# Kernel tuning notes

Measured on AMD Instinct MI355X. Metric: run time of the kernel, lower is better.

Reference implementation:

```python
import math
import jax, jax.numpy as jnp
import numpy as np

B, L, D = 2, 2048, 2048
H, DH = 16, 128
DFF = 8192


def setup_inputs() -> dict:
    key = jax.random.key(0)
    ks = jax.random.split(key, 9)
    x = jax.random.normal(ks[0], (B, L, D), dtype=jnp.float32)
    # additive causal mask: 0 on/below diagonal, -inf above
    neg = jnp.finfo(jnp.float32).min
    mask = jnp.where(jnp.tril(jnp.ones((L, L), dtype=bool)), 0.0, neg)[None, None]
    s = 0.02
    return {
        "x": x,
        "mask": mask,
        "ln1_w": jnp.ones((D,), jnp.float32),
        "wq": jax.random.normal(ks[1], (D, D), jnp.float32) * s,
        "wk": jax.random.normal(ks[2], (D, D), jnp.float32) * s,
        "wv": jax.random.normal(ks[3], (D, D), jnp.float32) * s,
        "wo": jax.random.normal(ks[4], (D, D), jnp.float32) * s,
        "ln2_w": jnp.ones((D,), jnp.float32),
        "w_up": jax.random.normal(ks[5], (DFF, D), jnp.float32) * s,
        "w_down": jax.random.normal(ks[6], (D, DFF), jnp.float32) * s,
    }


def _rmsnorm(x, w, eps=1e-8):
    rms = jnp.sqrt(jnp.mean(x * x, axis=-1, keepdims=True) + eps)
    return x / rms * w


def reference(x, mask, ln1_w, wq, wk, wv, wo, ln2_w, w_up, w_down):
    h = _rmsnorm(x, ln1_w)
    # torch Linear: y = x @ W.T ; weights are [out, in]
    q = (h @ wq.T).reshape(B, L, H, DH).transpose(0, 2, 1, 3)  # [B,H,L,DH]
    k = (h @ wk.T).reshape(B, L, H, DH).transpose(0, 2, 1, 3)
    v = (h @ wv.T).reshape(B, L, H, DH).transpose(0, 2, 1, 3)
    scores = jnp.einsum('bhqd,bhkd->bhqk', q, k) / math.sqrt(DH)
    scores = scores + mask
    attn = jax.nn.softmax(scores, axis=-1)
    out = jnp.einsum('bhqk,bhkd->bhqd', attn, v)
    out = out.transpose(0, 2, 1, 3).reshape(B, L, D)
    x = x + out @ wo.T
    h = _rmsnorm(x, ln2_w)
    ff = jax.nn.gelu(h @ w_up.T, approximate=False) @ w_down.T  # exact erf GELU as in F.gelu
    return x + ff
```

## Files before the change

### kernel.cpp

```cpp
#include <hip/hip_runtime.h>
#include <hip/hip_bf16.h>
#include <math.h>

#define B_   2
#define L_   2048
#define D_   2048
#define H_   16
#define DH_  128
#define DFF_ 8192
#define NTOK (B_*L_)

typedef __attribute__((ext_vector_type(8))) short bf16x8;
typedef __attribute__((ext_vector_type(4))) float floatx4;
typedef unsigned short u16;

__device__ __forceinline__ u16 f2bf(float f) {
    union { float f; unsigned u; } c; c.f = f;
    unsigned r = (c.u + 0x7fffu + ((c.u >> 16) & 1u)) >> 16;
    return (u16)r;
}

__device__ __forceinline__ void async_cp16(const u16* g, u16* l) {
    __builtin_amdgcn_global_load_lds(
        (const __attribute__((address_space(1))) unsigned int*)g,
        (__attribute__((address_space(3))) unsigned int*)l,
        16, 0, 0);
}

__global__ __launch_bounds__(256) void cvt_bf16(const float* __restrict__ in,
                                                u16* __restrict__ out, int n4) {
    int i = blockIdx.x * 256 + threadIdx.x;
    if (i >= n4) return;
    float4 v = ((const float4*)in)[i];
    ushort4 o = { f2bf(v.x), f2bf(v.y), f2bf(v.z), f2bf(v.w) };
    ((ushort4*)out)[i] = o;
}

__global__ __launch_bounds__(256) void rmsnorm_kernel(const float* __restrict__ x,
                                                      const float* __restrict__ w,
                                                      u16* __restrict__ out) {
    const int row = blockIdx.x, tid = threadIdx.x;
    const float* xr = x + (size_t)row * D_;
    float4 a = ((const float4*)xr)[tid];
    float4 b = ((const float4*)xr)[tid + 256];
    float ss = a.x*a.x + a.y*a.y + a.z*a.z + a.w*a.w
             + b.x*b.x + b.y*b.y + b.z*b.z + b.w*b.w;
#pragma unroll
    for (int d = 1; d < 64; d <<= 1) ss += __shfl_xor(ss, d, 64);
    __shared__ float sred[4];
    if ((tid & 63) == 0) sred[tid >> 6] = ss;
    __syncthreads();
    float tot = sred[0] + sred[1] + sred[2] + sred[3];
    float inv = 1.0f / sqrtf(tot * (1.0f / D_) + 1e-8f);
    float4 w0 = ((const float4*)w)[tid];
    float4 w1 = ((const float4*)w)[tid + 256];
    ushort4 o0 = { f2bf(a.x*inv*w0.x), f2bf(a.y*inv*w0.y), f2bf(a.z*inv*w0.z), f2bf(a.w*inv*w0.w) };
    ushort4 o1 = { f2bf(b.x*inv*w1.x), f2bf(b.y*inv*w1.y), f2bf(b.z*inv*w1.z), f2bf(b.w*inv*w1.w) };
    ushort4* orow = (ushort4*)(out + (size_t)row * D_);
    orow[tid] = o0;
    orow[tid + 256] = o1;
}


template<int MODE>
__global__ __launch_bounds__(512, 2) void gemm256(const u16* __restrict__ A,
                                                  const u16* __restrict__ Bw,
                                                  void* __restrict__ outp,
                                                  void* __restrict__ outp2,
                                                  const float* __restrict__ residual,
                                                  int M, int N, int K, float scale) {
    __shared__ __attribute__((aligned(16))) u16 lds_a[2][256 * 64];
    __shared__ __attribute__((aligned(16))) u16 lds_b[2][256 * 64];
    const int tid = threadIdx.x;
    const int wave = tid >> 6, lane = tid & 63;
    const int qd = lane >> 4, c16 = lane & 15;
    const int wm = wave >> 2, wn = wave & 3;
    const int gx = gridDim.x;
    const int nwg = gx * gridDim.y;
    const int orig = blockIdx.y * gx + blockIdx.x;
    const int id2 = (orig & 7) * (nwg >> 3) + (orig >> 3);
    const long tile_m = (long)(id2 / gx) * 256, tile_n = (long)(id2 % gx) * 256;
    const int NT = K >> 6;

    const int srow = tid >> 3;
    const int scol = (((tid & 7) ^ (srow & 7))) * 8;
    const u16* Asrc = A + (tile_m + srow) * (long)K + scol;
    const u16* Bsrc = Bw + (tile_n + srow) * (long)K + scol;
    const int stoff = tid * 8;

#define STAGE_A2(bi, g0, g1, ko) do { \
        async_cp16(Asrc + (long)(g0) * 64 * K + (ko), &lds_a[bi][(g0) * 4096 + stoff]); \
        async_cp16(Asrc + (long)(g1) * 64 * K + (ko), &lds_a[bi][(g1) * 4096 + stoff]); \
    } while (0)
#define STAGE_B2(bi, g0, g1, ko) do { \
        async_cp16(Bsrc + (long)(g0) * 64 * K + (ko), &lds_b[bi][(g0) * 4096 + stoff]); \
        async_cp16(Bsrc + (long)(g1) * 64 * K + (ko), &lds_b[bi][(g1) * 4096 + stoff]); \
    } while (0)

    const int csw = (qd * 16) ^ ((c16 & 7) << 4);
    const int arowb = (wm * 128 + c16) * 128;
    const int browb = (wn * 64 + c16) * 128;
#define LDAF(bi, i, ks) (*(const bf16x8*)((const char*)&lds_a[bi][0] + arowb + (i) * 2048 + (csw ^ ((ks) * 64))))
#define LDBF(bi, j, ks) (*(const bf16x8*)((const char*)&lds_b[bi][0] + browb + (j) * 2048 + (csw ^ ((ks) * 64))))
#define MFMA_(a, b, c) __builtin_amdgcn_mfma_f32_16x16x32_bf16(a, b, c, 0, 0, 0)

    floatx4 acc[8][4] = {};

    STAGE_B2(0, 0, 1, 0); STAGE_B2(0, 2, 3, 0);
    STAGE_A2(0, 0, 2, 0); STAGE_A2(0, 1, 3, 0);
    STAGE_B2(1, 0, 1, 64); STAGE_B2(1, 2, 3, 64);
    STAGE_A2(1, 0, 2, 64);
    asm volatile("s_waitcnt vmcnt(6)" ::: "memory");
    __builtin_amdgcn_s_barrier();
    asm volatile("" ::: "memory");

    bf16x8 bfr[4][2];

#define GP(bi, ip, STAGE, TAIL) do { \
        bf16x8 a0k0 = LDAF(bi, 2 * (ip), 0); \
        bf16x8 a0k1 = LDAF(bi, 2 * (ip), 1); \
        bf16x8 a1k0 = LDAF(bi, 2 * (ip) + 1, 0); \
        bf16x8 a1k1 = LDAF(bi, 2 * (ip) + 1, 1); \
        STAGE \
        __builtin_amdgcn_s_barrier(); \
        asm volatile("s_waitcnt lgkmcnt(0)" ::: "memory"); \
        __builtin_amdgcn_sched_barrier(0); \
        __builtin_amdgcn_s_setprio(1); \
        _Pragma("unroll") \
        for (int j = 0; j < 4; j++) { \
            acc[2 * (ip)][j]     = MFMA_(a0k0, bfr[j][0], acc[2 * (ip)][j]); \
            acc[2 * (ip)][j]     = MFMA_(a0k1, bfr[j][1], acc[2 * (ip)][j]); \
            acc[2 * (ip) + 1][j] = MFMA_(a1k0, bfr[j][0], acc[2 * (ip) + 1][j]); \
            acc[2 * (ip) + 1][j] = MFMA_(a1k1, bfr[j][1], acc[2 * (ip) + 1][j]); \
        } \
        __builtin_amdgcn_s_setprio(0); \
        __builtin_amdgcn_sched_barrier(0); \
        TAIL \
        __builtin_amdgcn_s_barrier(); \
        asm volatile("" ::: "memory"); \
    } while (0)

#define VMTAIL { if (s2) asm volatile("s_waitcnt vmcnt(6)" ::: "memory"); \
                 else    asm volatile("s_waitcnt vmcnt(0)" ::: "memory"); }

    for (int t = 0; t < NT; t += 2) {
        const int s2 = (t + 2) < NT;
        const long ko1 = (long)(t + 1) * 64;
        const long ko2 = (long)(t + 2) * 64;
        const long ko3 = (long)(t + 3) * 64;
#pragma unroll
        for (int j = 0; j < 4; j++) { bfr[j][0] = LDBF(0, j, 0); bfr[j][1] = LDBF(0, j, 1); }
        GP(0, 0, STAGE_A2(1, 1, 3, ko1);, );
        GP(0, 1, if (s2) STAGE_B2(0, 0, 1, ko2);, );
        GP(0, 2, if (s2) STAGE_B2(0, 2, 3, ko2);, );
        GP(0, 3, if (s2) STAGE_A2(0, 0, 2, ko2);, VMTAIL);
#pragma unroll
        for (int j = 0; j < 4; j++) { bfr[j][0] = LDBF(1, j, 0); bfr[j][1] = LDBF(1, j, 1); }
        GP(1, 0, if (s2) STAGE_A2(0, 1, 3, ko2);, );
        GP(1, 1, if (s2) STAGE_B2(1, 0, 1, ko3);, );
        GP(1, 2, if (s2) STAGE_B2(1, 2, 3, ko3);, );
        GP(1, 3, if (s2) STAGE_A2(1, 0, 2, ko3);, VMTAIL);
    }

#pragma unroll
    for (int i = 0; i < 8; i++) {
#pragma unroll
        for (int j = 0; j < 4; j++) {
#pragma unroll
            for (int r = 0; r < 4; r++) {
                long m = tile_m + wm * 128 + i * 16 + qd * 4 + r;
                long n = tile_n + wn * 64 + j * 16 + c16;
                float v = acc[i][j][r];
                if (MODE == 0) {
                    long b = m >> 11, l = m & 2047;
                    int isq = n < D_;
                    long f = n & 2047, h = f >> 7, dh = f & 127;
                    u16* dst = isq ? (u16*)outp : (u16*)outp2;
                    dst[((b * H_ + h) * (long)L_ + l) * DH_ + dh] =
                        f2bf(v * (isq ? scale : 1.0f));
                } else if (MODE == 1) {
                    long idx = m * (long)N + n;
                    ((float*)outp)[idx] = v + residual[idx];
                } else if (MODE == 2) {
                    float g = 0.5f * v * (1.0f + erff(v * 0.70710678118654752f));
                    ((u16*)outp)[m * (long)N + n] = f2bf(g);
                } else {
                    ((u16*)outp)[m * (long)N + n] = f2bf(v);
                }
            }
        }
    }
#undef GP
#undef VMTAIL
#undef STAGE_A2
#undef STAGE_B2
#undef LDAF
#undef LDBF
#undef MFMA_
}

template<int MODE>
__global__ __launch_bounds__(512, 2) void gemm128n(const u16* __restrict__ A,
                                                   const u16* __restrict__ Bw,
                                                   void* __restrict__ outp,
                                                   const float* __restrict__ residual,
                                                   int M, int N, int K) {
    __shared__ __attribute__((aligned(16))) u16 lds_a[2][128 * 64];
    __shared__ __attribute__((aligned(16))) u16 lds_b[2][256 * 64];
    const int tid = threadIdx.x;
    const int wave = tid >> 6, lane = tid & 63;
    const int qd = lane >> 4, c16 = lane & 15;
    const int wm = wave >> 2, wn = wave & 3;
    const int gx = gridDim.x;
    const int nwg = gx * gridDim.y;
    const int orig = blockIdx.y * gx + blockIdx.x;
    const int id2 = (orig & 7) * (nwg >> 3) + (orig >> 3);
    const long tile_m = (long)(id2 / gx) * 128, tile_n = (long)(id2 % gx) * 256;
    const int NT = K >> 6;

    const int srow = tid >> 3;
    const int scol = (((tid & 7) ^ (srow & 7))) * 8;
    const u16* Asrc = A + (tile_m + srow) * (long)K + scol;
    const u16* Bsrc = Bw + (tile_n + srow) * (long)K + scol;
    const int stoff = tid * 8;

#define STAGE_AA(bi, ko) do { \
        async_cp16(Asrc + (ko), &lds_a[bi][stoff]); \
        async_cp16(Asrc + 64 * (long)K + (ko), &lds_a[bi][4096 + stoff]); \
    } while (0)
#define STAGE_BA(bi, ko) do { \
        async_cp16(Bsrc + (ko), &lds_b[bi][stoff]); \
        async_cp16(Bsrc + 64 * (long)K + (ko), &lds_b[bi][4096 + stoff]); \
        async_cp16(Bsrc + 128 * (long)K + (ko), &lds_b[bi][8192 + stoff]); \
        async_cp16(Bsrc + 192 * (long)K + (ko), &lds_b[bi][12288 + stoff]); \
    } while (0)

    const int csw = (qd * 16) ^ ((c16 & 7) << 4);
    const int arowb = (wm * 64 + c16) * 128;
    const int browb = (wn * 64 + c16) * 128;
#define LDAF2(bi, i, ks) (*(const bf16x8*)((const char*)&lds_a[bi][0] + arowb + (i) * 2048 + (csw ^ ((ks) * 64))))
#define LDBF2(bi, j, ks) (*(const bf16x8*)((const char*)&lds_b[bi][0] + browb + (j) * 2048 + (csw ^ ((ks) * 64))))
#define MFMA_(a, b, c) __builtin_amdgcn_mfma_f32_16x16x32_bf16(a, b, c, 0, 0, 0)

    floatx4 acc[4][4] = {};

    STAGE_BA(0, 0); STAGE_AA(0, 0); STAGE_BA(1, 64);
    asm volatile("s_waitcnt vmcnt(4)" ::: "memory");
    __builtin_amdgcn_s_barrier();
    asm volatile("" ::: "memory");

    bf16x8 bfr[4][2];

#define GP2(bi, ip, STAGE, TAIL) do { \
        bf16x8 a0k0 = LDAF2(bi, 2 * (ip), 0); \
        bf16x8 a0k1 = LDAF2(bi, 2 * (ip), 1); \
        bf16x8 a1k0 = LDAF2(bi, 2 * (ip) + 1, 0); \
        bf16x8 a1k1 = LDAF2(bi, 2 * (ip) + 1, 1); \
        STAGE \
        __builtin_amdgcn_s_barrier(); \
        asm volatile("s_waitcnt lgkmcnt(0)" ::: "memory"); \
        __builtin_amdgcn_sched_barrier(0); \
        __builtin_amdgcn_s_setprio(1); \
        _Pragma("unroll") \
        for (int j = 0; j < 4; j++) { \
            acc[2 * (ip)][j]     = MFMA_(a0k0, bfr[j][0], acc[2 * (ip)][j]); \
            acc[2 * (ip)][j]     = MFMA_(a0k1, bfr[j][1], acc[2 * (ip)][j]); \
            acc[2 * (ip) + 1][j] = MFMA_(a1k0, bfr[j][0], acc[2 * (ip) + 1][j]); \
            acc[2 * (ip) + 1][j] = MFMA_(a1k1, bfr[j][1], acc[2 * (ip) + 1][j]); \
        } \
        __builtin_amdgcn_s_setprio(0); \
        __builtin_amdgcn_sched_barrier(0); \
        TAIL \
        __builtin_amdgcn_s_barrier(); \
        asm volatile("" ::: "memory"); \
    } while (0)

#define TILE2(tt, bi) do { \
        _Pragma("unroll") \
        for (int j = 0; j < 4; j++) { bfr[j][0] = LDBF2(bi, j, 0); bfr[j][1] = LDBF2(bi, j, 1); } \
        GP2(bi, 0, if ((tt) + 1 < NT) STAGE_AA(bi ^ 1, ((long)(tt) + 1) * 64);, ); \
        GP2(bi, 1, if ((tt) + 2 < NT) STAGE_BA(bi, ((long)(tt) + 2) * 64);, \
            { if ((tt) + 2 < NT) asm volatile("s_waitcnt vmcnt(4)" ::: "memory"); \
              else               asm volatile("s_waitcnt vmcnt(0)" ::: "memory"); }); \
    } while (0)

    for (int t = 0; t < NT; t += 2) {
        TILE2(t, 0);
        TILE2(t + 1, 1);
    }

#pragma unroll
    for (int i = 0; i < 4; i++) {
#pragma unroll
        for (int j = 0; j < 4; j++) {
#pragma unroll
            for (int r = 0; r < 4; r++) {
                long m = tile_m + wm * 64 + i * 16 + qd * 4 + r;
                long n = tile_n + wn * 64 + j * 16 + c16;
                float v = acc[i][j][r];
                if (MODE == 1) {
                    long idx = m * (long)N + n;
                    ((float*)outp)[idx] = v + residual[idx];
                } else {
                    ((u16*)outp)[m * (long)N + n] = f2bf(v);
                }
            }
        }
    }
#undef GP2
#undef TILE2
#undef STAGE_AA
#undef STAGE_BA
#undef LDAF2
#undef LDBF2
#undef MFMA_
}

#define KSTRIDE 136
#define VSTRIDE 72
#define PSTRIDE 72
__global__ __launch_bounds__(256) void attn_kernel(const u16* __restrict__ Q,
                                                   const u16* __restrict__ K,
                                                   const u16* __restrict__ VT,
                                                   u16* __restrict__ O) {
    __shared__ __attribute__((aligned(16))) u16 kt_lds[64 * KSTRIDE];
    __shared__ __attribute__((aligned(16))) u16 vt_lds[128 * VSTRIDE];
    __shared__ __attribute__((aligned(16))) u16 p_lds[4][16 * PSTRIDE];
    const int tid = threadIdx.x;
    const int wave = tid >> 6, lane = tid & 63;
    const int qd = lane >> 4, c16 = lane & 15;
    const int pair = blockIdx.x, bh = blockIdx.y;
    const int b = bh >> 4, h = bh & 15;
    const u16* qh = Q + (size_t)bh * L_ * DH_;
    const u16* kh = K + (size_t)bh * L_ * DH_;
    const u16* vth = VT + (size_t)h * DH_ * NTOK + (size_t)b * L_;

    for (int qsel = 0; qsel < 2; ++qsel) {
        const int qt = qsel ? (31 - pair) : pair;
        const int q0 = qt * 64;

        bf16x8 qf[4];
#pragma unroll
        for (int s = 0; s < 4; s++)
            qf[s] = *(const bf16x8*)(qh + (size_t)(q0 + wave * 16 + c16) * DH_ + s * 32 + qd * 8);

        floatx4 o_acc[8] = {};
        float m_i[4], l_i[4];
#pragma unroll
        for (int r = 0; r < 4; r++) { m_i[r] = -1e30f; l_i[r] = 0.f; }

        for (int kt = 0; kt <= qt; kt++) {
            const int kv0 = kt * 64;
#pragma unroll
            for (int s = 0; s < 4; s++) {
                int c = tid + s * 256;
                int kr = c >> 4, koff = (c & 15) * 8;
                *(int4*)&kt_lds[kr * KSTRIDE + koff] =
                    *(const int4*)(kh + (size_t)(kv0 + kr) * DH_ + koff);
                int dh = c >> 3, kv8 = (c & 7) * 8;
                *(int4*)&vt_lds[dh * VSTRIDE + kv8] =
                    *(const int4*)(vth + (size_t)dh * NTOK + kv0 + kv8);
            }
            __syncthreads();

            floatx4 s_acc[4] = {};
#pragma unroll
            for (int j = 0; j < 4; j++)
#pragma unroll
                for (int s = 0; s < 4; s++) {
                    bf16x8 kf = *(const bf16x8*)&kt_lds[(j * 16 + c16) * KSTRIDE + s * 32 + qd * 8];
                    s_acc[j] = __builtin_amdgcn_mfma_f32_16x16x32_bf16(qf[s], kf, s_acc[j], 0, 0, 0);
                }

            if (kt == qt) {
#pragma unroll
                for (int j = 0; j < 4; j++)
#pragma unroll
                    for (int r = 0; r < 4; r++) {
                        int col = j * 16 + c16;
                        int row = wave * 16 + qd * 4 + r;
                        if (col > row) s_acc[j][r] = -1e30f;
                    }
            }

            float rsum[4], alpha[4];
#pragma unroll
            for (int r = 0; r < 4; r++) {
                float mx = fmaxf(fmaxf(s_acc[0][r], s_acc[1][r]), fmaxf(s_acc[2][r], s_acc[3][r]));
#pragma unroll
                for (int d = 1; d < 16; d <<= 1) mx = fmaxf(mx, __shfl_xor(mx, d, 64));
                float mnew = fmaxf(m_i[r], mx);
                alpha[r] = __expf(m_i[r] - mnew);
                m_i[r] = mnew;
                rsum[r] = 0.f;
            }
#pragma unroll
            for (int j = 0; j < 4; j++)
#pragma unroll
                for (int r = 0; r < 4; r++) {
                    float p = __expf(s_acc[j][r] - m_i[r]);
                    s_acc[j][r] = p;
                    rsum[r] += p;
                }
#pragma unroll
            for (int r = 0; r < 4; r++) {
#pragma unroll
                for (int d = 1; d < 16; d <<= 1) rsum[r] += __shfl_xor(rsum[r], d, 64);
                l_i[r] = l_i[r] * alpha[r] + rsum[r];
            }
#pragma unroll
            for (int j8 = 0; j8 < 8; j8++)
#pragma unroll
                for (int r = 0; r < 4; r++) o_acc[j8][r] *= alpha[r];

#pragma unroll
            for (int j = 0; j < 4; j++)
#pragma unroll
                for (int r = 0; r < 4; r++)
                    p_lds[wave][(qd * 4 + r) * PSTRIDE + j * 16 + c16] = f2bf(s_acc[j][r]);

#pragma unroll
            for (int s = 0; s < 2; s++) {
                bf16x8 pf = *(const bf16x8*)&p_lds[wave][c16 * PSTRIDE + s * 32 + qd * 8];
#pragma unroll
                for (int j8 = 0; j8 < 8; j8++) {
                    bf16x8 vf = *(const bf16x8*)&vt_lds[(j8 * 16 + c16) * VSTRIDE + s * 32 + qd * 8];
                    o_acc[j8] = __builtin_amdgcn_mfma_f32_16x16x32_bf16(pf, vf, o_acc[j8], 0, 0, 0);
                }
            }
            __syncthreads();
        }

        float inv_l[4];
#pragma unroll
        for (int r = 0; r < 4; r++) inv_l[r] = 1.0f / l_i[r];
#pragma unroll
        for (int j8 = 0; j8 < 8; j8++)
#pragma unroll
            for (int r = 0; r < 4; r++) {
                int l = q0 + wave * 16 + qd * 4 + r;
                int d = h * DH_ + j8 * 16 + c16;
                O[(size_t)(b * L_ + l) * D_ + d] = f2bf(o_acc[j8][r] * inv_l[r]);
            }
    }
}

extern "C" void kernel_launch(void* const* d_in, const int* in_sizes, int n_in,
                              void* d_out, int out_size, void* d_ws, size_t ws_size,
                              hipStream_t stream) {
    const float* x     = (const float*)d_in[0];
    const float* ln1_w = (const float*)d_in[2];
    const float* wq    = (const float*)d_in[3];
    const float* wk    = (const float*)d_in[4];
    const float* wv    = (const float*)d_in[5];
    const float* wo    = (const float*)d_in[6];
    const float* ln2_w = (const float*)d_in[7];
    const float* w_up  = (const float*)d_in[8];
    const float* w_dn  = (const float*)d_in[9];

    char* ws = (char*)d_ws;
    const size_t MB = 1024 * 1024;
    float* x2   = (float*)(ws + 0);
    u16* hbuf   = (u16*)(ws + 32 * MB);
    u16* qbuf   = (u16*)(ws + 48 * MB);
    u16* kbuf   = (u16*)(ws + 64 * MB);
    u16* vtbuf  = (u16*)(ws + 80 * MB);
    u16* attnb  = (u16*)(ws + 96 * MB);
    u16* upbuf  = (u16*)(ws + 48 * MB);
    u16* wbufA  = (u16*)(ws + 112 * MB);
    u16* wbufC  = (u16*)(ws + 128 * MB);

    dim3 blk(256), blk512(512);
    const int nW = D_ * D_;
    const int nU = DFF_ * D_;
    cvt_bf16<<<(nW / 4 + 255) / 256, blk, 0, stream>>>(wq, wbufA, nW / 4);
    cvt_bf16<<<(nW / 4 + 255) / 256, blk, 0, stream>>>(wk, wbufA + (size_t)nW, nW / 4);
    cvt_bf16<<<(nW / 4 + 255) / 256, blk, 0, stream>>>(wv, wbufC, nW / 4);
    rmsnorm_kernel<<<NTOK, blk, 0, stream>>>(x, ln1_w, hbuf);

    gemm256<0><<<dim3(2 * D_ / 256, NTOK / 256), blk512, 0, stream>>>(
        hbuf, wbufA, qbuf, kbuf, nullptr, NTOK, 2 * D_, D_, 0.08838834764831845f);
    gemm128n<3><<<dim3(NTOK / 256, D_ / 128), blk512, 0, stream>>>(
        wbufC, hbuf, vtbuf, nullptr, D_, NTOK, D_);

    dim3 ga(16, B_ * H_);
    attn_kernel<<<ga, blk, 0, stream>>>(qbuf, kbuf, vtbuf, attnb);

    cvt_bf16<<<(nW / 4 + 255) / 256, blk, 0, stream>>>(wo, wbufA, nW / 4);
    gemm128n<1><<<dim3(D_ / 256, NTOK / 128), blk512, 0, stream>>>(
        attnb, wbufA, x2, x, NTOK, D_, D_);

    rmsnorm_kernel<<<NTOK, blk, 0, stream>>>(x2, ln2_w, hbuf);

    cvt_bf16<<<(nU / 4 + 255) / 256, blk, 0, stream>>>(w_up, wbufA, nU / 4);
    gemm256<2><<<dim3(DFF_ / 256, NTOK / 256), blk512, 0, stream>>>(
        hbuf, wbufA, upbuf, nullptr, nullptr, NTOK, DFF_, D_, 1.0f);

    cvt_bf16<<<(nU / 4 + 255) / 256, blk, 0, stream>>>(w_dn, wbufA, nU / 4);
    gemm128n<1><<<dim3(D_ / 256, NTOK / 128), blk512, 0, stream>>>(
        upbuf, wbufA, (float*)d_out, x2, NTOK, D_, DFF_);
}
```

Before: 792.6 us.

## Software-pipeline A-fragment LDS reads ahead of MFMA phases in GEMM kernels

Restructures the inner loops of both GEMM kernels so the next A-fragment LDS reads are issued before the current MFMA phase, using double-buffered register fragments (afA/afB). It also drops the explicit lgkmcnt(0) wait and sched_barriers, leaving the compiler to order waits. The goal is to hide LDS read latency behind MFMA work and remove one barrier per phase. In exchange it raises register pressure and makes correctness depend on compiler-inserted waits and on barrier placement relative to buffer overwrites.

```diff
diff --git a/kernel.cpp b/kernel.cpp
--- a/kernel.cpp
+++ b/kernel.cpp
@@ -104,7 +104,28 @@
 #define LDBF(bi, j, ks) (*(const bf16x8*)((const char*)&lds_b[bi][0] + browb + (j) * 2048 + (csw ^ ((ks) * 64))))
 #define MFMA_(a, b, c) __builtin_amdgcn_mfma_f32_16x16x32_bf16(a, b, c, 0, 0, 0)
 
+#define READ_BFR(bi) do { \
+        _Pragma("unroll") \
+        for (int j = 0; j < 4; j++) { bfr[j][0] = LDBF(bi, j, 0); bfr[j][1] = LDBF(bi, j, 1); } \
+    } while (0)
+#define READ_AF(dst, bi, r0) do { \
+        dst[0] = LDAF(bi, r0, 0); dst[1] = LDAF(bi, r0, 1); \
+        dst[2] = LDAF(bi, (r0) + 1, 0); dst[3] = LDAF(bi, (r0) + 1, 1); \
+    } while (0)
+#define MFMA_PH(af, R) do { \
+        __builtin_amdgcn_s_setprio(1); \
+        _Pragma("unroll") \
+        for (int j = 0; j < 4; j++) { \
+            acc[R][j]       = MFMA_(af[0], bfr[j][0], acc[R][j]); \
+            acc[R][j]       = MFMA_(af[1], bfr[j][1], acc[R][j]); \
+            acc[(R) + 1][j] = MFMA_(af[2], bfr[j][0], acc[(R) + 1][j]); \
+            acc[(R) + 1][j] = MFMA_(af[3], bfr[j][1], acc[(R) + 1][j]); \
+        } \
+        __builtin_amdgcn_s_setprio(0); \
+    } while (0)
+
     floatx4 acc[8][4] = {};
+    bf16x8 bfr[4][2];
 
     STAGE_B2(0, 0, 1, 0); STAGE_B2(0, 2, 3, 0);
     STAGE_A2(0, 0, 2, 0); STAGE_A2(0, 1, 3, 0);
@@ -112,54 +133,41 @@
     STAGE_A2(1, 0, 2, 64);
     asm volatile("s_waitcnt vmcnt(6)" ::: "memory");
     __builtin_amdgcn_s_barrier();
-    asm volatile("" ::: "memory");
-
-    bf16x8 bfr[4][2];
-
-#define GP(bi, ip, STAGE, TAIL) do { \
-        bf16x8 a0k0 = LDAF(bi, 2 * (ip), 0); \
-        bf16x8 a0k1 = LDAF(bi, 2 * (ip), 1); \
-        bf16x8 a1k0 = LDAF(bi, 2 * (ip) + 1, 0); \
-        bf16x8 a1k1 = LDAF(bi, 2 * (ip) + 1, 1); \
-        STAGE \
+
+#define TILE256(bi, koN, koNN, GA1, GS) do { \
+        READ_BFR(bi); \
+        bf16x8 afA[4], afB[4]; \
+        READ_AF(afA, bi, 0); \
+         \
+        READ_AF(afB, bi, 2); \
+        if (GA1) STAGE_A2((bi) ^ 1, 1, 3, koN); \
+        MFMA_PH(afA, 0); \
         __builtin_amdgcn_s_barrier(); \
-        asm volatile("s_waitcnt lgkmcnt(0)" ::: "memory"); \
-        __builtin_amdgcn_sched_barrier(0); \
-        __builtin_amdgcn_s_setprio(1); \
-        _Pragma("unroll") \
-        for (int j = 0; j < 4; j++) { \
-            acc[2 * (ip)][j]     = MFMA_(a0k0, bfr[j][0], acc[2 * (ip)][j]); \
-            acc[2 * (ip)][j]     = MFMA_(a0k1, bfr[j][1], acc[2 * (ip)][j]); \
-            acc[2 * (ip) + 1][j] = MFMA_(a1k0, bfr[j][0], acc[2 * (ip) + 1][j]); \
-            acc[2 * (ip) + 1][j] = MFMA_(a1k1, bfr[j][1], acc[2 * (ip) + 1][j]); \
-        } \
-        __builtin_amdgcn_s_setprio(0); \
-        __builtin_amdgcn_sched_barrier(0); \
-        TAIL \
+         \
+        READ_AF(afA, bi, 4); \
+        if (GS) STAGE_B2(bi, 0, 1, koNN); \
+        MFMA_PH(afB, 2); \
         __builtin_amdgcn_s_barrier(); \
-        asm volatile("" ::: "memory"); \
-    } while (0)
-
-#define VMTAIL { if (s2) asm volatile("s_waitcnt vmcnt(6)" ::: "memory"); \
-                 else    asm volatile("s_waitcnt vmcnt(0)" ::: "memory"); }
+         \
+        READ_AF(afB, bi, 6); \
+        if (GS) STAGE_B2(bi, 2, 3, koNN); \
+        MFMA_PH(afA, 4); \
+        __builtin_amdgcn_s_barrier(); \
+         \
+        if (GS) STAGE_A2(bi, 0, 2, koNN); \
+        MFMA_PH(afB, 6); \
+        if (GS) asm volatile("s_waitcnt vmcnt(6)" ::: "memory"); \
+        else    asm volatile("s_waitcnt vmcnt(0)" ::: "memory"); \
+        __builtin_amdgcn_s_barrier(); \
+    } while (0)
 
     for (int t = 0; t < NT; t += 2) {
         const int s2 = (t + 2) < NT;
         const long ko1 = (long)(t + 1) * 64;
         const long ko2 = (long)(t + 2) * 64;
         const long ko3 = (long)(t + 3) * 64;
-#pragma unroll
-        for (int j = 0; j < 4; j++) { bfr[j][0] = LDBF(0, j, 0); bfr[j][1] = LDBF(0, j, 1); }
-        GP(0, 0, STAGE_A2(1, 1, 3, ko1);, );
-        GP(0, 1, if (s2) STAGE_B2(0, 0, 1, ko2);, );
-        GP(0, 2, if (s2) STAGE_B2(0, 2, 3, ko2);, );
-        GP(0, 3, if (s2) STAGE_A2(0, 0, 2, ko2);, VMTAIL);
-#pragma unroll
-        for (int j = 0; j < 4; j++) { bfr[j][0] = LDBF(1, j, 0); bfr[j][1] = LDBF(1, j, 1); }
-        GP(1, 0, if (s2) STAGE_A2(0, 1, 3, ko2);, );
-        GP(1, 1, if (s2) STAGE_B2(1, 0, 1, ko3);, );
-        GP(1, 2, if (s2) STAGE_B2(1, 2, 3, ko3);, );
-        GP(1, 3, if (s2) STAGE_A2(1, 0, 2, ko3);, VMTAIL);
+        TILE256(0, ko1, ko2, 1, s2);
+        TILE256(1, ko2, ko3, s2, s2);
     }
 
 #pragma unroll
@@ -190,8 +198,10 @@
             }
         }
     }
-#undef GP
-#undef VMTAIL
+#undef TILE256
+#undef READ_BFR
+#undef READ_AF
+#undef MFMA_PH
 #undef STAGE_A2
 #undef STAGE_B2
 #undef LDAF
@@ -242,51 +252,57 @@
 #define LDBF2(bi, j, ks) (*(const bf16x8*)((const char*)&lds_b[bi][0] + browb + (j) * 2048 + (csw ^ ((ks) * 64))))
 #define MFMA_(a, b, c) __builtin_amdgcn_mfma_f32_16x16x32_bf16(a, b, c, 0, 0, 0)
 
+#define READ_BFR2(bi) do { \
+        _Pragma("unroll") \
+        for (int j = 0; j < 4; j++) { bfr[j][0] = LDBF2(bi, j, 0); bfr[j][1] = LDBF2(bi, j, 1); } \
+    } while (0)
+#define READ_AF2(dst, bi, r0) do { \
+        dst[0] = LDAF2(bi, r0, 0); dst[1] = LDAF2(bi, r0, 1); \
+        dst[2] = LDAF2(bi, (r0) + 1, 0); dst[3] = LDAF2(bi, (r0) + 1, 1); \
+    } while (0)
+#define MFMA_PH2(af, R) do { \
+        __builtin_amdgcn_s_setprio(1); \
+        _Pragma("unroll") \
+        for (int j = 0; j < 4; j++) { \
+            acc[R][j]       = MFMA_(af[0], bfr[j][0], acc[R][j]); \
+            acc[R][j]       = MFMA_(af[1], bfr[j][1], acc[R][j]); \
+            acc[(R) + 1][j] = MFMA_(af[2], bfr[j][0], acc[(R) + 1][j]); \
+            acc[(R) + 1][j] = MFMA_(af[3], bfr[j][1], acc[(R) + 1][j]); \
+        } \
+        __builtin_amdgcn_s_setprio(0); \
+    } while (0)
+
     floatx4 acc[4][4] = {};
+    bf16x8 bfr[4][2];
 
     STAGE_BA(0, 0); STAGE_AA(0, 0); STAGE_BA(1, 64);
     asm volatile("s_waitcnt vmcnt(4)" ::: "memory");
     __builtin_amdgcn_s_barrier();
-    asm volatile("" ::: "memory");
-
-    bf16x8 bfr[4][2];
-
-#define GP2(bi, ip, STAGE, TAIL) do { \
-        bf16x8 a0k0 = LDAF2(bi, 2 * (ip), 0); \
-        bf16x8 a0k1 = LDAF2(bi, 2 * (ip), 1); \
-        bf16x8 a1k0 = LDAF2(bi, 2 * (ip) + 1, 0); \
-        bf16x8 a1k1 = LDAF2(bi, 2 * (ip) + 1, 1); \
-        STAGE \
+
+#define TILE128(bi, koN, koNN, GA1, GS) do { \
+        READ_BFR2(bi); \
+        bf16x8 afA[4], afB[4]; \
+        READ_AF2(afA, bi, 0); \
+         \
+        READ_AF2(afB, bi, 2); \
+        if (GA1) STAGE_AA((bi) ^ 1, koN); \
+        MFMA_PH2(afA, 0); \
         __builtin_amdgcn_s_barrier(); \
-        asm volatile("s_waitcnt lgkmcnt(0)" ::: "memory"); \
-        __builtin_amdgcn_sched_barrier(0); \
-        __builtin_amdgcn_s_setprio(1); \
-        _Pragma("unroll") \
-        for (int j = 0; j < 4; j++) { \
-            acc[2 * (ip)][j]     = MFMA_(a0k0, bfr[j][0], acc[2 * (ip)][j]); \
-            acc[2 * (ip)][j]     = MFMA_(a0k1, bfr[j][1], acc[2 * (ip)][j]); \
-            acc[2 * (ip) + 1][j] = MFMA_(a1k0, bfr[j][0], acc[2 * (ip) + 1][j]); \
-            acc[2 * (ip) + 1][j] = MFMA_(a1k1, bfr[j][1], acc[2 * (ip) + 1][j]); \
-        } \
-        __builtin_amdgcn_s_setprio(0); \
-        __builtin_amdgcn_sched_barrier(0); \
-        TAIL \
+         \
+        if (GS) STAGE_BA(bi, koNN); \
+        MFMA_PH2(afB, 2); \
+        if (GS) asm volatile("s_waitcnt vmcnt(4)" ::: "memory"); \
+        else    asm volatile("s_waitcnt vmcnt(0)" ::: "memory"); \
         __builtin_amdgcn_s_barrier(); \
-        asm volatile("" ::: "memory"); \
-    } while (0)
-
-#define TILE2(tt, bi) do { \
-        _Pragma("unroll") \
-        for (int j = 0; j < 4; j++) { bfr[j][0] = LDBF2(bi, j, 0); bfr[j][1] = LDBF2(bi, j, 1); } \
-        GP2(bi, 0, if ((tt) + 1 < NT) STAGE_AA(bi ^ 1, ((long)(tt) + 1) * 64);, ); \
-        GP2(bi, 1, if ((tt) + 2 < NT) STAGE_BA(bi, ((long)(tt) + 2) * 64);, \
-            { if ((tt) + 2 < NT) asm volatile("s_waitcnt vmcnt(4)" ::: "memory"); \
-              else               asm volatile("s_waitcnt vmcnt(0)" ::: "memory"); }); \
     } while (0)
 
     for (int t = 0; t < NT; t += 2) {
-        TILE2(t, 0);
-        TILE2(t + 1, 1);
+        const int g1 = (t + 1) < NT, s2 = (t + 2) < NT;
+        const long ko1 = (long)(t + 1) * 64;
+        const long ko2 = (long)(t + 2) * 64;
+        const long ko3 = (long)(t + 3) * 64;
+        TILE128(0, ko1, ko2, g1, s2);
+        TILE128(1, ko2, ko3, s2, s2);
     }
 
 #pragma unroll
@@ -307,8 +323,10 @@
             }
         }
     }
-#undef GP2
-#undef TILE2
+#undef TILE128
+#undef READ_BFR2
+#undef READ_AF2
+#undef MFMA_PH2
 #undef STAGE_AA
 #undef STAGE_BA
 #undef LDAF2
```

Result: faster. 766.0 us (-3.4%).
